# Kernel optimization log

Measured on AMD Instinct MI355X. Metric: run time of the kernel, lower is better.

Reference implementation:

```python
import jax, jax.numpy as jnp
import numpy as np

IGNORE_INDEX = 255
LOSS_WEIGHT = 1.0


def _flow_warp_nearest(img, flow):
    """mmcv.flow_warp with default interpolate_mode='nearest', filling_value=0.
    img: (C, H, W) float, flow: (H, W, 2) with flow[...,0]=dx, flow[...,1]=dy.
    output[:, y, x] = img[:, round(y+dy), round(x+dx)], 0 outside bounds.
    """
    C, H, W = img.shape
    ys = jnp.arange(H, dtype=flow.dtype)[:, None] + flow[..., 1]  # (H, W)
    xs = jnp.arange(W, dtype=flow.dtype)[None, :] + flow[..., 0]  # (H, W)
    ry = jnp.round(ys).astype(jnp.int32)
    rx = jnp.round(xs).astype(jnp.int32)
    valid = (ry >= 0) & (ry < H) & (rx >= 0) & (rx < W)
    ryc = jnp.clip(ry, 0, H - 1)
    rxc = jnp.clip(rx, 0, W - 1)
    warped = img[:, ryc, rxc]  # gather -> (C, H, W)
    return jnp.where(valid[None, :, :], warped, jnp.zeros((), img.dtype))


def setup_inputs() -> dict:
    key = jax.random.key(0)
    k1, k2, k3, k4 = jax.random.split(key, 4)
    B, C, H, W = 4, 19, 512, 1024
    preds = jax.random.normal(k1, (B, C, H, W), dtype=jnp.float32)
    targets = jax.random.normal(k2, (B, C, H, W), dtype=jnp.float32)
    opt_flow = jax.random.normal(k3, (B, 1, H, W, 2), dtype=jnp.float32)
    gt_labels = jax.random.randint(k4, (B, H, W), 0, 19, dtype=jnp.int64)
    return {"preds": preds, "targets": targets, "opt_flow": opt_flow,
            "gt_labels": gt_labels}


def reference(preds, targets, opt_flow, gt_labels):
    # softmax over class dim
    p = jax.nn.softmax(preds, axis=1)    # (B, C, H, W)
    t = jax.nn.softmax(targets, axis=1)  # (B, C, H, W)
    flow = opt_flow[:, 0]                # (B, H, W, 2), the per-sample squeeze(0)
    # per-sample optical-flow warp of predictions (detached in the original)
    pw = jax.vmap(_flow_warp_nearest)(p, flow)
    pw = jax.lax.stop_gradient(pw)
    # temporal mIoU
    non_ignore = (gt_labels != IGNORE_INDEX).astype(t.dtype)[:, None]  # (B,1,H,W)
    t = t * non_ignore
    num = jnp.sum(jnp.abs(pw * t), axis=(2, 3))            # (B, C)
    den = jnp.sum(jnp.abs(pw + t - pw * t), axis=(2, 3))   # (B, C)
    num_classes = t.shape[1]
    miou = jnp.sum(num / den, axis=1) / num_classes        # (B,)
    loss = 1.0 - miou
    return LOSS_WEIGHT * jnp.mean(loss)  # reduction='mean'
```

## Files before the change

kernel.cpp:

```cpp
#include <hip/hip_runtime.h>

#define HH 512
#define WW 1024
#define NC 19
#define HWP (HH * WW)
#define NB 4
#define NREP 4
#define NXCD 8
#define IGNORE_IDX 255

typedef float f2v __attribute__((ext_vector_type(2)));

__global__ __launch_bounds__(256) void tc_main(
    const float* __restrict__ preds,
    const float* __restrict__ targets,
    const float* __restrict__ flow,
    const int* __restrict__ labels,
    float* __restrict__ acc)
{
    const int tid = threadIdx.x;

    const int nwg   = gridDim.x;
    const int chunk = nwg / NXCD;
    const int phys  = blockIdx.x;
    const int logical = (phys % NXCD) * chunk + phys / NXCD;

    const int blocks_per_img = nwg / NB;
    const int b   = logical / blocks_per_img;
    const int blk = logical % blocks_per_img;

    float accn[NC];
    float accd[NC];
#pragma unroll
    for (int c = 0; c < NC; ++c) { accn[c] = 0.f; accd[c] = 0.f; }

    const float* tb = targets + (size_t)b * NC * HWP;
    const float* pb = preds   + (size_t)b * NC * HWP;
    const f2v*   fb = (const f2v*)(flow + (size_t)b * HWP * 2);
    const int*   lb = labels  + (size_t)b * HWP;

    const int per_block = HWP / blocks_per_img;
    const int base = blk * per_block;

    for (int k = tid; k < per_block; k += blockDim.x) {
        const int pix = base + k;
        const int y = pix >> 10;
        const int x = pix & (WW - 1);

        const f2v f = __builtin_nontemporal_load(&fb[pix]);
        const float fx = (float)x + f.x;
        const float fy = (float)y + f.y;
        const int rx = (int)rintf(fx);
        const int ry = (int)rintf(fy);
        const bool valid = (rx >= 0) && (rx < WW) && (ry >= 0) && (ry < HH);
        const int rxc = min(max(rx, 0), WW - 1);
        const int ryc = min(max(ry, 0), HH - 1);
        const int spix = ryc * WW + rxc;

        const bool keep = (__builtin_nontemporal_load(&lb[pix]) != IGNORE_IDX);

        float te[NC];
        float tsum = 0.f;
#pragma unroll
        for (int c = 0; c < NC; ++c) {
            te[c] = __expf(__builtin_nontemporal_load(&tb[(size_t)c * HWP + pix]));
            tsum += te[c];
        }
        const float tinv = keep ? (1.0f / tsum) : 0.0f;

        float pe[NC];
        float psum = 0.f;
#pragma unroll
        for (int c = 0; c < NC; ++c) {
            pe[c] = __expf(pb[(size_t)c * HWP + spix]);
            psum += pe[c];
        }
        const float pinv = valid ? (1.0f / psum) : 0.0f;

#pragma unroll
        for (int c = 0; c < NC; ++c) {
            const float t = te[c] * tinv;
            const float p = pe[c] * pinv;
            const float pt = p * t;
            accn[c] += pt;
            accd[c] += p + t - pt;
        }
    }

#pragma unroll
    for (int c = 0; c < NC; ++c) {
        for (int off = 32; off > 0; off >>= 1) {
            accn[c] += __shfl_xor(accn[c], off);
            accd[c] += __shfl_xor(accd[c], off);
        }
    }

    __shared__ float s[4][NC][2];
    const int wave = tid >> 6;
    const int lane = tid & 63;
    if (lane == 0) {
#pragma unroll
        for (int c = 0; c < NC; ++c) {
            s[wave][c][0] = accn[c];
            s[wave][c][1] = accd[c];
        }
    }
    __syncthreads();
    if (tid < NC * 2) {
        const int c = tid >> 1;
        const int which = tid & 1;
        const float v = s[0][c][which] + s[1][c][which] + s[2][c][which] + s[3][c][which];
        const int rep = phys & (NREP - 1);
        atomicAdd(&acc[(((size_t)rep * NB + b) * NC + c) * 2 + which], v);
    }
}

__global__ void tc_final(const float* __restrict__ acc, float* __restrict__ out)
{
    if (threadIdx.x == 0 && blockIdx.x == 0) {
        float total = 0.f;
        for (int b = 0; b < NB; ++b) {
            float m = 0.f;
            for (int c = 0; c < NC; ++c) {
                float n = 0.f, d = 0.f;
                for (int r = 0; r < NREP; ++r) {
                    n += acc[(((size_t)r * NB + b) * NC + c) * 2 + 0];
                    d += acc[(((size_t)r * NB + b) * NC + c) * 2 + 1];
                }
                m += n / d;
            }
            total += 1.0f - m / (float)NC;
        }
        out[0] = total / (float)NB;
    }
}

extern "C" void kernel_launch(void* const* d_in, const int* in_sizes, int n_in,
                              void* d_out, int out_size, void* d_ws, size_t ws_size,
                              hipStream_t stream) {
    const float* preds   = (const float*)d_in[0];
    const float* targets = (const float*)d_in[1];
    const float* flow    = (const float*)d_in[2];
    const int*   labels  = (const int*)d_in[3];
    float* acc = (float*)d_ws;

    hipMemsetAsync(acc, 0, (size_t)NREP * NB * NC * 2 * sizeof(float), stream);

    tc_main<<<2048, 256, 0, stream>>>(preds, targets, flow, labels, acc);
    tc_final<<<1, 64, 0, stream>>>(acc, (float*)d_out);
}
```

Before: 103.5 us.

## Split class channels across wave pairs with shared-memory softmax sum exchange

Each block now covers 128 pixels per iteration instead of 256. Two waves handle the first 10 classes and two waves handle the remaining 9 for the same pixels, and each pair swaps its partial exp sums through double-buffered shared memory with a block barrier on every iteration. This roughly halves the per-thread register arrays and accumulators, which should lower register pressure and allow higher occupancy for latency hiding on the gather loads. In exchange, the flow and label loads are duplicated across the two halves and a __syncthreads is added every iteration.

```diff
diff --git a/kernel.cpp b/kernel.cpp
--- a/kernel.cpp
+++ b/kernel.cpp
@@ -11,6 +11,40 @@
 
 typedef float f2v __attribute__((ext_vector_type(2)));
 
+template<int C0, int NCH>
+__device__ __forceinline__ void half_load(
+    const float* __restrict__ tb, const float* __restrict__ pb,
+    int pix, int spix, float (&te)[10], float (&pe)[10],
+    float& ts, float& ps)
+{
+    ts = 0.f; ps = 0.f;
+#pragma unroll
+    for (int i = 0; i < NCH; ++i) {
+        te[i] = __expf(__builtin_nontemporal_load(&tb[(size_t)(C0 + i) * HWP + pix]));
+        ts += te[i];
+    }
+#pragma unroll
+    for (int i = 0; i < NCH; ++i) {
+        pe[i] = __expf(pb[(size_t)(C0 + i) * HWP + spix]);
+        ps += pe[i];
+    }
+}
+
+template<int NCH>
+__device__ __forceinline__ void half_acc(
+    const float (&te)[10], const float (&pe)[10],
+    float tinv, float pinv, float (&accn)[10], float (&accd)[10])
+{
+#pragma unroll
+    for (int i = 0; i < NCH; ++i) {
+        const float t = te[i] * tinv;
+        const float p = pe[i] * pinv;
+        const float pt = p * t;
+        accn[i] += pt;
+        accd[i] += p + t - pt;
+    }
+}
+
 __global__ __launch_bounds__(256) void tc_main(
     const float* __restrict__ preds,
     const float* __restrict__ targets,
@@ -18,7 +52,11 @@
     const int* __restrict__ labels,
     float* __restrict__ acc)
 {
-    const int tid = threadIdx.x;
+    const int tid   = threadIdx.x;
+    const int w     = tid >> 6;
+    const int lane  = tid & 63;
+    const int chalf = w >> 1;
+    const int pl    = ((w & 1) << 6) | lane;
 
     const int nwg   = gridDim.x;
     const int chunk = nwg / NXCD;
@@ -29,89 +67,73 @@
     const int b   = logical / blocks_per_img;
     const int blk = logical % blocks_per_img;
 
-    float accn[NC];
-    float accd[NC];
-#pragma unroll
-    for (int c = 0; c < NC; ++c) { accn[c] = 0.f; accd[c] = 0.f; }
-
     const float* tb = targets + (size_t)b * NC * HWP;
     const float* pb = preds   + (size_t)b * NC * HWP;
     const f2v*   fb = (const f2v*)(flow + (size_t)b * HWP * 2);
     const int*   lb = labels  + (size_t)b * HWP;
 
     const int per_block = HWP / blocks_per_img;
-    const int base = blk * per_block;
+    const int base  = blk * per_block;
+    const int nIter = per_block / 128;
 
-    for (int k = tid; k < per_block; k += blockDim.x) {
-        const int pix = base + k;
+    __shared__ float2 part[2][2][128];
+    __shared__ float  sred[4][10][2];
+
+    float accn[10], accd[10];
+#pragma unroll
+    for (int i = 0; i < 10; ++i) { accn[i] = 0.f; accd[i] = 0.f; }
+
+    for (int it = 0; it < nIter; ++it) {
+        const int pix = base + it * 128 + pl;
         const int y = pix >> 10;
         const int x = pix & (WW - 1);
 
         const f2v f = __builtin_nontemporal_load(&fb[pix]);
-        const float fx = (float)x + f.x;
-        const float fy = (float)y + f.y;
-        const int rx = (int)rintf(fx);
-        const int ry = (int)rintf(fy);
+        const int rx = (int)rintf((float)x + f.x);
+        const int ry = (int)rintf((float)y + f.y);
         const bool valid = (rx >= 0) && (rx < WW) && (ry >= 0) && (ry < HH);
-        const int rxc = min(max(rx, 0), WW - 1);
-        const int ryc = min(max(ry, 0), HH - 1);
-        const int spix = ryc * WW + rxc;
-
+        const int spix = min(max(ry, 0), HH - 1) * WW + min(max(rx, 0), WW - 1);
         const bool keep = (__builtin_nontemporal_load(&lb[pix]) != IGNORE_IDX);
 
-        float te[NC];
-        float tsum = 0.f;
-#pragma unroll
-        for (int c = 0; c < NC; ++c) {
-            te[c] = __expf(__builtin_nontemporal_load(&tb[(size_t)c * HWP + pix]));
-            tsum += te[c];
-        }
-        const float tinv = keep ? (1.0f / tsum) : 0.0f;
+        float te[10], pe[10], ts, ps;
+        if (chalf == 0) half_load<0, 10>(tb, pb, pix, spix, te, pe, ts, ps);
+        else            half_load<10, 9>(tb, pb, pix, spix, te, pe, ts, ps);
 
-        float pe[NC];
-        float psum = 0.f;
-#pragma unroll
-        for (int c = 0; c < NC; ++c) {
-            pe[c] = __expf(pb[(size_t)c * HWP + spix]);
-            psum += pe[c];
-        }
-        const float pinv = valid ? (1.0f / psum) : 0.0f;
+        const int buf = it & 1;
+        part[buf][chalf][pl] = make_float2(ts, ps);
+        __syncthreads();
+        const float2 o = part[buf][1 - chalf][pl];
 
-#pragma unroll
-        for (int c = 0; c < NC; ++c) {
-            const float t = te[c] * tinv;
-            const float p = pe[c] * pinv;
-            const float pt = p * t;
-            accn[c] += pt;
-            accd[c] += p + t - pt;
-        }
+        const float tinv = keep  ? (1.0f / (ts + o.x)) : 0.0f;
+        const float pinv = valid ? (1.0f / (ps + o.y)) : 0.0f;
+
+        if (chalf == 0) half_acc<10>(te, pe, tinv, pinv, accn, accd);
+        else            half_acc<9>(te, pe, tinv, pinv, accn, accd);
     }
 
 #pragma unroll
-    for (int c = 0; c < NC; ++c) {
+    for (int i = 0; i < 10; ++i) {
         for (int off = 32; off > 0; off >>= 1) {
-            accn[c] += __shfl_xor(accn[c], off);
-            accd[c] += __shfl_xor(accd[c], off);
+            accn[i] += __shfl_xor(accn[i], off);
+            accd[i] += __shfl_xor(accd[i], off);
         }
     }
-
-    __shared__ float s[4][NC][2];
-    const int wave = tid >> 6;
-    const int lane = tid & 63;
     if (lane == 0) {
 #pragma unroll
-        for (int c = 0; c < NC; ++c) {
-            s[wave][c][0] = accn[c];
-            s[wave][c][1] = accd[c];
+        for (int i = 0; i < 10; ++i) {
+            sred[w][i][0] = accn[i];
+            sred[w][i][1] = accd[i];
         }
     }
     __syncthreads();
     if (tid < NC * 2) {
-        const int c = tid >> 1;
-        const int which = tid & 1;
-        const float v = s[0][c][which] + s[1][c][which] + s[2][c][which] + s[3][c][which];
+        const int c  = tid >> 1;
+        const int wh = tid & 1;
+        float v;
+        if (c < 10) v = sred[0][c][wh] + sred[1][c][wh];
+        else        v = sred[2][c - 10][wh] + sred[3][c - 10][wh];
         const int rep = phys & (NREP - 1);
-        atomicAdd(&acc[(((size_t)rep * NB + b) * NC + c) * 2 + which], v);
+        atomicAdd(&acc[(((size_t)rep * NB + b) * NC + c) * 2 + wh], v);
     }
 }
 
```

Measured after the change: 106.7 us. 3.2% more time.

## Precompute fp16 pixel-major softmax records for preds before warped gather

Applied to the files above, without the earlier changes.

Adds a prep kernel that computes the softmax of preds once per pixel and stores the 19 probabilities as fp16 in a 48-byte pixel-major record in the workspace. The main kernel then gathers one contiguous record per warped pixel instead of 19 strided loads from separate class planes, and skips the exp and normalisation on the gathered side. This trades extra global write and read traffic plus an extra launch for a cheaper, more coalesced gather. It also lowers prediction precision to fp16. A fallback to the original fused kernel is kept for when the workspace is too small.

```diff
diff --git a/kernel.cpp b/kernel.cpp
--- a/kernel.cpp
+++ b/kernel.cpp
@@ -8,10 +8,142 @@
 #define NREP 4
 #define NXCD 8
 #define IGNORE_IDX 255
+#define RECB 48
 
 typedef float f2v __attribute__((ext_vector_type(2)));
-
-__global__ __launch_bounds__(256) void tc_main(
+typedef float f4v __attribute__((ext_vector_type(4)));
+typedef _Float16 h16;
+
+union Rec { f4v v[3]; h16 h[24]; };
+
+__global__ __launch_bounds__(256) void tc_prep(
+    const float* __restrict__ preds, char* __restrict__ P)
+{
+    const int t = blockIdx.x * 256 + threadIdx.x;
+    const int pix2 = t * 2;
+    const int b   = pix2 >> 19;
+    const int pix = pix2 & (HWP - 1);
+    const float* pb = preds + (size_t)b * NC * HWP + pix;
+
+    float e0[NC], e1[NC];
+    float s0 = 0.f, s1 = 0.f;
+#pragma unroll
+    for (int c = 0; c < NC; ++c) {
+        const f2v v = __builtin_nontemporal_load((const f2v*)(pb + (size_t)c * HWP));
+        e0[c] = __expf(v.x); s0 += e0[c];
+        e1[c] = __expf(v.y); s1 += e1[c];
+    }
+    const float i0 = 1.f / s0, i1 = 1.f / s1;
+
+    const f4v zero = {0.f, 0.f, 0.f, 0.f};
+    Rec r0, r1;
+#pragma unroll
+    for (int i = 0; i < 3; ++i) { r0.v[i] = zero; r1.v[i] = zero; }
+#pragma unroll
+    for (int c = 0; c < NC; ++c) {
+        r0.h[c] = (h16)(e0[c] * i0);
+        r1.h[c] = (h16)(e1[c] * i1);
+    }
+    f4v* out = (f4v*)(P + (size_t)pix2 * RECB);
+    out[0] = r0.v[0]; out[1] = r0.v[1]; out[2] = r0.v[2];
+    out[3] = r1.v[0]; out[4] = r1.v[1]; out[5] = r1.v[2];
+}
+
+__global__ __launch_bounds__(256) void tc_main_p(
+    const char* __restrict__ P,
+    const float* __restrict__ targets,
+    const float* __restrict__ flow,
+    const int* __restrict__ labels,
+    float* __restrict__ acc)
+{
+    const int tid = threadIdx.x;
+
+    const int nwg   = gridDim.x;
+    const int chunk = nwg / NXCD;
+    const int phys  = blockIdx.x;
+    const int logical = (phys % NXCD) * chunk + phys / NXCD;
+
+    const int blocks_per_img = nwg / NB;
+    const int b   = logical / blocks_per_img;
+    const int blk = logical % blocks_per_img;
+
+    float accn[NC], accd[NC];
+#pragma unroll
+    for (int c = 0; c < NC; ++c) { accn[c] = 0.f; accd[c] = 0.f; }
+
+    const float* tb = targets + (size_t)b * NC * HWP;
+    const char*  Pb = P + (size_t)b * HWP * RECB;
+    const f2v*   fb = (const f2v*)(flow + (size_t)b * HWP * 2);
+    const int*   lb = labels + (size_t)b * HWP;
+
+    const int per_block = HWP / blocks_per_img;
+    const int base = blk * per_block;
+
+    for (int k = tid; k < per_block; k += 256) {
+        const int pix = base + k;
+        const int y = pix >> 10;
+        const int x = pix & (WW - 1);
+
+        const f2v f = __builtin_nontemporal_load(&fb[pix]);
+        const int rx = (int)rintf((float)x + f.x);
+        const int ry = (int)rintf((float)y + f.y);
+        const bool valid = (rx >= 0) && (rx < WW) && (ry >= 0) && (ry < HH);
+        const int spix = min(max(ry, 0), HH - 1) * WW + min(max(rx, 0), WW - 1);
+        const bool keep = (__builtin_nontemporal_load(&lb[pix]) != IGNORE_IDX);
+
+        Rec r;
+        const f4v* rec = (const f4v*)(Pb + (size_t)spix * RECB);
+        r.v[0] = rec[0]; r.v[1] = rec[1]; r.v[2] = rec[2];
+        const float validf = valid ? 1.f : 0.f;
+
+        float te[NC];
+        float tsum = 0.f;
+#pragma unroll
+        for (int c = 0; c < NC; ++c) {
+            te[c] = __expf(__builtin_nontemporal_load(&tb[(size_t)c * HWP + pix]));
+            tsum += te[c];
+        }
+        const float tinv = keep ? (1.0f / tsum) : 0.0f;
+
+#pragma unroll
+        for (int c = 0; c < NC; ++c) {
+            const float t = te[c] * tinv;
+            const float p = (float)r.h[c] * validf;
+            const float pt = p * t;
+            accn[c] += pt;
+            accd[c] += p + t - pt;
+        }
+    }
+
+#pragma unroll
+    for (int c = 0; c < NC; ++c) {
+        for (int off = 32; off > 0; off >>= 1) {
+            accn[c] += __shfl_xor(accn[c], off);
+            accd[c] += __shfl_xor(accd[c], off);
+        }
+    }
+
+    __shared__ float s[4][NC][2];
+    const int wave = tid >> 6;
+    const int lane = tid & 63;
+    if (lane == 0) {
+#pragma unroll
+        for (int c = 0; c < NC; ++c) {
+            s[wave][c][0] = accn[c];
+            s[wave][c][1] = accd[c];
+        }
+    }
+    __syncthreads();
+    if (tid < NC * 2) {
+        const int c = tid >> 1;
+        const int which = tid & 1;
+        const float v = s[0][c][which] + s[1][c][which] + s[2][c][which] + s[3][c][which];
+        const int rep = phys & (NREP - 1);
+        atomicAdd(&acc[(((size_t)rep * NB + b) * NC + c) * 2 + which], v);
+    }
+}
+
+__global__ __launch_bounds__(256) void tc_main_direct(
     const float* __restrict__ preds,
     const float* __restrict__ targets,
     const float* __restrict__ flow,
@@ -19,18 +151,15 @@
     float* __restrict__ acc)
 {
     const int tid = threadIdx.x;
-
     const int nwg   = gridDim.x;
     const int chunk = nwg / NXCD;
     const int phys  = blockIdx.x;
     const int logical = (phys % NXCD) * chunk + phys / NXCD;
-
     const int blocks_per_img = nwg / NB;
     const int b   = logical / blocks_per_img;
     const int blk = logical % blocks_per_img;
 
-    float accn[NC];
-    float accd[NC];
+    float accn[NC], accd[NC];
 #pragma unroll
     for (int c = 0; c < NC; ++c) { accn[c] = 0.f; accd[c] = 0.f; }
 
@@ -42,41 +171,31 @@
     const int per_block = HWP / blocks_per_img;
     const int base = blk * per_block;
 
-    for (int k = tid; k < per_block; k += blockDim.x) {
+    for (int k = tid; k < per_block; k += 256) {
         const int pix = base + k;
         const int y = pix >> 10;
         const int x = pix & (WW - 1);
-
         const f2v f = __builtin_nontemporal_load(&fb[pix]);
-        const float fx = (float)x + f.x;
-        const float fy = (float)y + f.y;
-        const int rx = (int)rintf(fx);
-        const int ry = (int)rintf(fy);
+        const int rx = (int)rintf((float)x + f.x);
+        const int ry = (int)rintf((float)y + f.y);
         const bool valid = (rx >= 0) && (rx < WW) && (ry >= 0) && (ry < HH);
-        const int rxc = min(max(rx, 0), WW - 1);
-        const int ryc = min(max(ry, 0), HH - 1);
-        const int spix = ryc * WW + rxc;
-
+        const int spix = min(max(ry, 0), HH - 1) * WW + min(max(rx, 0), WW - 1);
         const bool keep = (__builtin_nontemporal_load(&lb[pix]) != IGNORE_IDX);
 
-        float te[NC];
-        float tsum = 0.f;
+        float te[NC], pe[NC];
+        float tsum = 0.f, psum = 0.f;
 #pragma unroll
         for (int c = 0; c < NC; ++c) {
             te[c] = __expf(__builtin_nontemporal_load(&tb[(size_t)c * HWP + pix]));
             tsum += te[c];
         }
-        const float tinv = keep ? (1.0f / tsum) : 0.0f;
-
-        float pe[NC];
-        float psum = 0.f;
 #pragma unroll
         for (int c = 0; c < NC; ++c) {
             pe[c] = __expf(pb[(size_t)c * HWP + spix]);
             psum += pe[c];
         }
+        const float tinv = keep  ? (1.0f / tsum) : 0.0f;
         const float pinv = valid ? (1.0f / psum) : 0.0f;
-
 #pragma unroll
         for (int c = 0; c < NC; ++c) {
             const float t = te[c] * tinv;
@@ -94,16 +213,12 @@
             accd[c] += __shfl_xor(accd[c], off);
         }
     }
-
     __shared__ float s[4][NC][2];
     const int wave = tid >> 6;
     const int lane = tid & 63;
     if (lane == 0) {
 #pragma unroll
-        for (int c = 0; c < NC; ++c) {
-            s[wave][c][0] = accn[c];
-            s[wave][c][1] = accd[c];
-        }
+        for (int c = 0; c < NC; ++c) { s[wave][c][0] = accn[c]; s[wave][c][1] = accd[c]; }
     }
     __syncthreads();
     if (tid < NC * 2) {
@@ -146,6 +261,15 @@
 
     hipMemsetAsync(acc, 0, (size_t)NREP * NB * NC * 2 * sizeof(float), stream);
 
-    tc_main<<<2048, 256, 0, stream>>>(preds, targets, flow, labels, acc);
+    const size_t pbytes = (size_t)NB * HWP * RECB;
+    const size_t need   = 1024 + pbytes;
+
+    if (ws_size >= need) {
+        char* P = (char*)d_ws + 1024;
+        tc_prep<<<(NB * HWP / 2) / 256, 256, 0, stream>>>(preds, P);
+        tc_main_p<<<2048, 256, 0, stream>>>(P, targets, flow, labels, acc);
+    } else {
+        tc_main_direct<<<2048, 256, 0, stream>>>(preds, targets, flow, labels, acc);
+    }
     tc_final<<<1, 64, 0, stream>>>(acc, (float*)d_out);
 }
```

New measurement: 142.6 us. +37.9%, slower.

## Tile pixels into 32x16 blocks and batch warped-pred gathers ahead of target loads

Applied to the files above, without the earlier changes.

Each workgroup now covers a 32-row by 16-column pixel tile instead of a contiguous row segment, and the grid grows to 4096 blocks with two pixels per thread. All 38 gather loads of warped predictions are issued together before the target loads, so more memory traffic is in flight. The exponentials are kept packed as fp16 pairs to save registers. The 2D tile is meant to make flow-gather accesses more local in cache, but the 16-wide columns coalesce worse for target loads, and fp16 storage of the exponentials adds rounding error (and overflow for large logits).

```diff
diff --git a/kernel.cpp b/kernel.cpp
--- a/kernel.cpp
+++ b/kernel.cpp
@@ -8,8 +8,20 @@
 #define NREP 4
 #define NXCD 8
 #define IGNORE_IDX 255
+#define TRW 32
+#define TCL 16
 
 typedef float f2v __attribute__((ext_vector_type(2)));
+
+__device__ __forceinline__ unsigned pack_h2(float a, float b) {
+    unsigned short lo = __builtin_bit_cast(unsigned short, (_Float16)a);
+    unsigned short hi = __builtin_bit_cast(unsigned short, (_Float16)b);
+    return (unsigned)lo | ((unsigned)hi << 16);
+}
+__device__ __forceinline__ float unpack_h2(unsigned v, int j) {
+    unsigned short u = (unsigned short)(j ? (v >> 16) : (v & 0xffff));
+    return (float)__builtin_bit_cast(_Float16, u);
+}
 
 __global__ __launch_bounds__(256) void tc_main(
     const float* __restrict__ preds,
@@ -25,38 +37,57 @@
     const int phys  = blockIdx.x;
     const int logical = (phys % NXCD) * chunk + phys / NXCD;
 
-    const int blocks_per_img = nwg / NB;
-    const int b   = logical / blocks_per_img;
-    const int blk = logical % blocks_per_img;
-
-    float accn[NC];
-    float accd[NC];
-#pragma unroll
-    for (int c = 0; c < NC; ++c) { accn[c] = 0.f; accd[c] = 0.f; }
+    const int b   = logical >> 10;
+    const int il  = logical & 1023;
+    const int tr  = il >> 6;
+    const int tc  = il & 63;
+    const int row0 = tr * TRW;
+    const int col0 = tc * TCL;
 
     const float* tb = targets + (size_t)b * NC * HWP;
     const float* pb = preds   + (size_t)b * NC * HWP;
     const f2v*   fb = (const f2v*)(flow + (size_t)b * HWP * 2);
     const int*   lb = labels  + (size_t)b * HWP;
 
-    const int per_block = HWP / blocks_per_img;
-    const int base = blk * per_block;
+    int   sp[2];
+    float vf[2];
+    int   pixg[2];
 
-    for (int k = tid; k < per_block; k += blockDim.x) {
-        const int pix = base + k;
-        const int y = pix >> 10;
-        const int x = pix & (WW - 1);
+#pragma unroll
+    for (int j = 0; j < 2; ++j) {
+        const int pi  = j * 256 + tid;
+        const int r   = row0 + (pi >> 4);
+        const int c_  = col0 + (pi & (TCL - 1));
+        const int pix = r * WW + c_;
+        pixg[j] = pix;
 
         const f2v f = __builtin_nontemporal_load(&fb[pix]);
-        const float fx = (float)x + f.x;
-        const float fy = (float)y + f.y;
-        const int rx = (int)rintf(fx);
-        const int ry = (int)rintf(fy);
+        const int rx = (int)rintf((float)c_ + f.x);
+        const int ry = (int)rintf((float)r  + f.y);
         const bool valid = (rx >= 0) && (rx < WW) && (ry >= 0) && (ry < HH);
-        const int rxc = min(max(rx, 0), WW - 1);
-        const int ryc = min(max(ry, 0), HH - 1);
-        const int spix = ryc * WW + rxc;
+        sp[j] = min(max(ry, 0), HH - 1) * WW + min(max(rx, 0), WW - 1);
+        vf[j] = valid ? 1.f : 0.f;
+    }
 
+    float psum0 = 0.f, psum1 = 0.f;
+    unsigned pe2[NC];
+#pragma unroll
+    for (int c = 0; c < NC; ++c) {
+        const float e0 = __expf(pb[(size_t)c * HWP + sp[0]]);
+        const float e1 = __expf(pb[(size_t)c * HWP + sp[1]]);
+        psum0 += e0;
+        psum1 += e1;
+        pe2[c] = pack_h2(e0, e1);
+    }
+    const float pinv[2] = { vf[0] / psum0, vf[1] / psum1 };
+
+    float accn[NC], accd[NC];
+#pragma unroll
+    for (int c = 0; c < NC; ++c) { accn[c] = 0.f; accd[c] = 0.f; }
+
+#pragma unroll
+    for (int j = 0; j < 2; ++j) {
+        const int pix = pixg[j];
         const bool keep = (__builtin_nontemporal_load(&lb[pix]) != IGNORE_IDX);
 
         float te[NC];
@@ -67,20 +98,12 @@
             tsum += te[c];
         }
         const float tinv = keep ? (1.0f / tsum) : 0.0f;
-
-        float pe[NC];
-        float psum = 0.f;
-#pragma unroll
-        for (int c = 0; c < NC; ++c) {
-            pe[c] = __expf(pb[(size_t)c * HWP + spix]);
-            psum += pe[c];
-        }
-        const float pinv = valid ? (1.0f / psum) : 0.0f;
+        const float pv   = pinv[j];
 
 #pragma unroll
         for (int c = 0; c < NC; ++c) {
             const float t = te[c] * tinv;
-            const float p = pe[c] * pinv;
+            const float p = unpack_h2(pe2[c], j) * pv;
             const float pt = p * t;
             accn[c] += pt;
             accd[c] += p + t - pt;
@@ -146,6 +169,6 @@
 
     hipMemsetAsync(acc, 0, (size_t)NREP * NB * NC * 2 * sizeof(float), stream);
 
-    tc_main<<<2048, 256, 0, stream>>>(preds, targets, flow, labels, acc);
+    tc_main<<<4096, 256, 0, stream>>>(preds, targets, flow, labels, acc);
     tc_final<<<1, 64, 0, stream>>>(acc, (float*)d_out);
 }
```

Result: slower. 114.9 us (+11.1%).
